# Kernel tuning notes

Hardware: AMD Instinct MI355X
Metric: run time of the kernel (lower is better)

## Reference

```python
import jax, jax.numpy as jnp
import numpy as np
import math

B, S, H, M, NH = 4, 1024, 1024, 32768, 1  # batch, seq, hidden, memory_size, num_heads


def setup_inputs() -> dict:
    key = jax.random.key(0)
    ks = jax.random.split(key, 12)
    init = lambda k, shape: (jax.random.normal(k, shape, dtype=jnp.float32) * 0.02)
    return {
        "hidden_states": jax.random.normal(ks[0], (B, S, H), dtype=jnp.float32),
        "Wq": init(ks[1], (H, H)), "bq": jnp.zeros((H,), jnp.float32),
        "Wk": init(ks[2], (H, H)), "bk": jnp.zeros((H,), jnp.float32),
        "Wv": init(ks[3], (H, H)), "bv": jnp.zeros((H,), jnp.float32),
        "Wo": init(ks[4], (H, H)), "bo": jnp.zeros((H,), jnp.float32),
        "memory_keys": init(ks[5], (NH, M, H)),
        "memory_values": init(ks[6], (NH, M, H)),
        "memory_age": jnp.zeros((NH, M), jnp.float32),
    }


def reference(hidden_states, Wq, bq, Wk, bk, Wv, bv, Wo, bo,
              memory_keys, memory_values, memory_age):
    b, s, _ = hidden_states.shape
    # projections (torch Linear: x @ W.T + b), split into heads
    q = (hidden_states @ Wq.T + bq).reshape(b, s, NH, -1)
    k = (hidden_states @ Wk.T + bk).reshape(b, s, NH, -1)
    v = (hidden_states @ Wv.T + bv).reshape(b, s, NH, -1)

    # cross-attention to external memory: [b,s,h,m]
    scores = jnp.einsum('bshd,hmd->bshm', q, memory_keys) / math.sqrt(H)
    probs = jax.nn.softmax(scores, axis=-1)  # dropout is identity (eval / p used deterministically)
    mem_out = jnp.einsum('bshm,hmd->bshd', probs, memory_values)

    # --- memory update (LRU-style topk scatter) ---
    age = memory_age + 1.0                       # [h,m]
    importance = probs.sum(axis=(0, 1))          # [h,m]
    _, upd_idx = jax.lax.top_k(age + (1.0 - importance), s)  # [h, s]
    h_idx = jnp.arange(NH)[:, None]              # [h,1]
    src_k = k[0, -1][:, None, :]                 # [h,1,d] -> broadcast over s slots
    src_v = v[0, -1][:, None, :]
    new_keys = memory_keys.at[h_idx, upd_idx].set(src_k)
    new_values = memory_values.at[h_idx, upd_idx].set(src_v)
    new_age = age.at[h_idx, upd_idx].set(0.0)

    output = mem_out.reshape(b, s, -1) @ Wo.T + bo

    access_counts = jnp.sum(probs > 0.01, axis=(0, 1))          # [h,m]
    max_scores = jnp.max(scores, axis=-1).mean()
    memory_usage = jnp.mean((new_age > 0).astype(jnp.float32))
    return (output, access_counts, max_scores, memory_usage,
            new_keys, new_values, new_age)
```

## Files before the change

kernel.cpp:

```cpp
#include <hip/hip_runtime.h>

#define SCALE 0.03125f
#define BAND_EPS 1e-6
#define BAND_CAP 8192
#define RB 4
#define NCHUNK 8

typedef unsigned int u32;
typedef unsigned short u16;
typedef unsigned long long u64;
typedef __attribute__((ext_vector_type(8))) short bf16x8;
typedef __attribute__((ext_vector_type(4))) float f32x4;

#define MFMA16(A,B,C) __builtin_amdgcn_mfma_f32_16x16x32_bf16(A,B,C,0,0,0)

__device__ __forceinline__ u32 fenc(float x){ u32 u=__float_as_uint(x); return (u&0x80000000u)? ~u : (u|0x80000000u); }
__device__ __forceinline__ float fdec(u32 e){ return (e&0x80000000u)? __uint_as_float(e&0x7FFFFFFFu) : __uint_as_float(~e); }
__device__ __forceinline__ u16 f2bf(float f){ u32 u=__float_as_uint(f); u32 r=(u + 0x7FFFu + ((u>>16)&1u))>>16; return (u16)r; }
__device__ __forceinline__ float bf2f(u16 h){ return __uint_as_float(((u32)h)<<16); }

__device__ __forceinline__ uint4 nt_load16(const void* p){
  const u64* q = (const u64*)p;
  u64 lo = __builtin_nontemporal_load(q);
  u64 hi = __builtin_nontemporal_load(q+1);
  uint4 r;
  r.x = (u32)lo; r.y = (u32)(lo>>32);
  r.z = (u32)hi; r.w = (u32)(hi>>32);
  return r;
}

__global__ __launch_bounds__(256) void k_projq64(const float* __restrict__ X, const float* __restrict__ W,
    const float* __restrict__ bias, float* __restrict__ Qhi, u16* __restrict__ Qh, u16* __restrict__ Ql)
{
  __shared__ float Xs[16][68], Ws[16][68];
  int t=threadIdx.x, ty=t>>4, tx=t&15;
  int row0=blockIdx.y*64, col0=blockIdx.x*64;
  int lr=t>>2, lk=(t&3)*4;
  double acc[4][4]={};
  for (int k0=0;k0<1024;k0+=16){
    __syncthreads();
    {
      float4 x = *(const float4*)(X + (size_t)(row0+lr)*1024 + k0 + lk);
      float4 w = *(const float4*)(W + (size_t)(col0+lr)*1024 + k0 + lk);
      Xs[lk+0][lr]=x.x; Xs[lk+1][lr]=x.y; Xs[lk+2][lr]=x.z; Xs[lk+3][lr]=x.w;
      Ws[lk+0][lr]=w.x; Ws[lk+1][lr]=w.y; Ws[lk+2][lr]=w.z; Ws[lk+3][lr]=w.w;
    }
    __syncthreads();
    #pragma unroll
    for (int kk=0;kk<16;kk++){
      double a[4], b[4];
      #pragma unroll
      for (int i=0;i<4;i++) a[i] = (double)Xs[kk][ty*4+i];
      #pragma unroll
      for (int j=0;j<4;j++) b[j] = (double)Ws[kk][tx*4+j];
      #pragma unroll
      for (int i=0;i<4;i++)
        #pragma unroll
        for (int j=0;j<4;j++)
          acc[i][j] = fma(a[i], b[j], acc[i][j]);
    }
  }
  #pragma unroll
  for (int i=0;i<4;i++)
    #pragma unroll
    for (int j=0;j<4;j++){
      double q = acc[i][j] + (double)bias[col0+tx*4+j];
      float hi = (float)q;
      size_t off = (size_t)(row0+ty*4+i)*1024 + col0 + tx*4 + j;
      Qhi[off] = hi;
      if (Qh){
        u16 h = f2bf(hi);
        Qh[off] = h;
        if (Ql) Ql[off] = f2bf(hi - bf2f(h));
      }
    }
}

__global__ __launch_bounds__(256) void k_rowproj(const float* __restrict__ hs,
    const float* __restrict__ Wk, const float* __restrict__ bk,
    const float* __restrict__ Wv, const float* __restrict__ bv,
    float* __restrict__ krow, float* __restrict__ vrow)
{
  int b = blockIdx.x; int which = b >> 10; int o = b & 1023; int t = threadIdx.x;
  const float* W = which ? Wv : Wk;
  const float* bias = which ? bv : bk;
  const float* x = hs + (size_t)1023*1024;
  double s = 0;
  for (int k=t;k<1024;k+=256) s += (double)x[k] * (double)W[(size_t)o*1024+k];
  __shared__ double sd[256];
  sd[t]=s; __syncthreads();
  for (int off=128;off>0;off>>=1){ if(t<off) sd[t]+=sd[t+off]; __syncthreads(); }
  if (t==0){ float* dst = which? vrow : krow; dst[o] = (float)(sd[0] + (double)bias[o]); }
}

__global__ __launch_bounds__(256) void k_cvt_mk(const float* __restrict__ src, u16* __restrict__ dst)
{
  size_t base = ((size_t)blockIdx.x*256 + threadIdx.x) * 16;
  float v[16];
  #pragma unroll
  for (int q=0;q<4;q++) *(float4*)&v[q*4] = *(const float4*)(src + base + q*4);
  u16 h[16];
  #pragma unroll
  for (int q=0;q<16;q++) h[q] = f2bf(v[q]);
  *(uint4*)(dst+base)   = *(uint4*)&h[0];
  *(uint4*)(dst+base+8) = *(uint4*)&h[8];
}

__global__ __launch_bounds__(256) void k_cvt_mvt(const float* __restrict__ MV, u32* __restrict__ MVT)
{
  size_t mp = blockIdx.x; int d = threadIdx.x*4;
  float4 r0 = *(const float4*)(MV + (2*mp  )*1024 + d);
  float4 r1 = *(const float4*)(MV + (2*mp+1)*1024 + d);
  u32 o[4];
  o[0] = (u32)f2bf(r0.x) | ((u32)f2bf(r1.x)<<16);
  o[1] = (u32)f2bf(r0.y) | ((u32)f2bf(r1.y)<<16);
  o[2] = (u32)f2bf(r0.z) | ((u32)f2bf(r1.z)<<16);
  o[3] = (u32)f2bf(r0.w) | ((u32)f2bf(r1.w)<<16);
  *(uint4*)(MVT + mp*1024 + d) = *(uint4*)o;
}

template<bool SPLIT>
__device__ __forceinline__ void sweep_core(
    const float* __restrict__ Qg, const float* __restrict__ MKg,
    int row0, int col0,
    u16 (*Ah)[40], u16 (*Al)[40], u16 (*Bh)[40],
    f32x4 acc[2][8])
{
  int t = threadIdx.x;
  int w = t >> 6, g = (t >> 4) & 3, c = t & 15;
  int srow = t >> 1, sq = (t & 1) * 16;
  const float* xg = Qg  + (size_t)(row0 + srow)*1024 + sq;
  const float* wg = MKg + (size_t)(col0 + srow)*1024 + sq;
  float xr[16], wr[16];
  #pragma unroll
  for (int q=0;q<4;q++){
    *(float4*)&xr[q*4] = *(const float4*)(xg + q*4);
    *(float4*)&wr[q*4] = *(const float4*)(wg + q*4);
  }
  for (int k0 = 0; k0 < 1024; k0 += 32){
    u16 ah[16], al[16], bh[16];
    #pragma unroll
    for (int q=0;q<16;q++){
      u16 h = f2bf(xr[q]); ah[q]=h;
      bh[q] = f2bf(wr[q]);
      if constexpr (SPLIT) al[q]=f2bf(xr[q]-bf2f(h));
    }
    __syncthreads();
    *(uint4*)&Ah[srow][sq]   = *(uint4*)&ah[0];
    *(uint4*)&Ah[srow][sq+8] = *(uint4*)&ah[8];
    *(uint4*)&Bh[srow][sq]   = *(uint4*)&bh[0];
    *(uint4*)&Bh[srow][sq+8] = *(uint4*)&bh[8];
    if constexpr (SPLIT){
      *(uint4*)&Al[srow][sq]   = *(uint4*)&al[0];
      *(uint4*)&Al[srow][sq+8] = *(uint4*)&al[8];
    }
    __syncthreads();
    if (k0 + 32 < 1024){
      #pragma unroll
      for (int q=0;q<4;q++){
        *(float4*)&xr[q*4] = *(const float4*)(xg + k0+32 + q*4);
        *(float4*)&wr[q*4] = *(const float4*)(wg + k0+32 + q*4);
      }
    }
    bf16x8 afh[2], afl[2];
    #pragma unroll
    for (int fi=0; fi<2; fi++){
      afh[fi] = *(const bf16x8*)&Ah[w*32 + fi*16 + c][g*8];
      if constexpr (SPLIT) afl[fi] = *(const bf16x8*)&Al[w*32 + fi*16 + c][g*8];
    }
    #pragma unroll
    for (int fj=0; fj<8; fj++){
      bf16x8 bfh = *(const bf16x8*)&Bh[fj*16 + c][g*8];
      #pragma unroll
      for (int fi=0; fi<2; fi++){
        acc[fi][fj] = MFMA16(afh[fi], bfh, acc[fi][fj]);
        if constexpr (SPLIT)
          acc[fi][fj] = MFMA16(afl[fi], bfh, acc[fi][fj]);
      }
    }
  }
}

template<bool SPLIT>
__device__ __forceinline__ void sweep_core_pre(
    const u16* __restrict__ Ag, const u16* __restrict__ Alg, const u16* __restrict__ Bg,
    int row0, int col0,
    u16 (*Ah)[40], u16 (*Al)[40], u16 (*Bh)[40],
    f32x4 acc[2][8])
{
  int t = threadIdx.x;
  int w = t >> 6, g = (t >> 4) & 3, c = t & 15;
  int srow = t >> 1, sq = (t & 1) * 16;
  const u16* xa = Ag + (size_t)(row0+srow)*1024 + sq;
  const u16* wb = Bg + (size_t)(col0+srow)*1024 + sq;
  const u16* xl = Alg + (size_t)(row0+srow)*1024 + sq;
  uint4 a0 = *(const uint4*)xa, a1 = *(const uint4*)(xa+8);
  uint4 b0 = *(const uint4*)wb, b1 = *(const uint4*)(wb+8);
  uint4 l0, l1;
  if constexpr (SPLIT){ l0 = *(const uint4*)xl; l1 = *(const uint4*)(xl+8); }
  for (int k0 = 0; k0 < 1024; k0 += 32){
    __syncthreads();
    *(uint4*)&Ah[srow][sq]   = a0;
    *(uint4*)&Ah[srow][sq+8] = a1;
    *(uint4*)&Bh[srow][sq]   = b0;
    *(uint4*)&Bh[srow][sq+8] = b1;
    if constexpr (SPLIT){
      *(uint4*)&Al[srow][sq]   = l0;
      *(uint4*)&Al[srow][sq+8] = l1;
    }
    __syncthreads();
    if (k0 + 32 < 1024){
      a0=*(const uint4*)(xa+k0+32); a1=*(const uint4*)(xa+k0+40);
      b0=*(const uint4*)(wb+k0+32); b1=*(const uint4*)(wb+k0+40);
      if constexpr (SPLIT){ l0=*(const uint4*)(xl+k0+32); l1=*(const uint4*)(xl+k0+40); }
    }
    bf16x8 afh[2], afl[2];
    #pragma unroll
    for (int fi=0; fi<2; fi++){
      afh[fi] = *(const bf16x8*)&Ah[w*32 + fi*16 + c][g*8];
      if constexpr (SPLIT) afl[fi] = *(const bf16x8*)&Al[w*32 + fi*16 + c][g*8];
    }
    #pragma unroll
    for (int fj=0; fj<8; fj++){
      bf16x8 bfh = *(const bf16x8*)&Bh[fj*16 + c][g*8];
      #pragma unroll
      for (int fi=0; fi<2; fi++){
        acc[fi][fj] = MFMA16(afh[fi], bfh, acc[fi][fj]);
        if constexpr (SPLIT)
          acc[fi][fj] = MFMA16(afl[fi], bfh, acc[fi][fj]);
      }
    }
  }
}

__device__ __forceinline__ void sweep1_epi(f32x4 acc[2][8], int row0,
    double* Zrow, u32* rmk)
{
  int t=threadIdx.x, w=t>>6, g=(t>>4)&3, c=t&15;
  #pragma unroll
  for (int fi=0;fi<2;fi++){
    #pragma unroll
    for (int r=0;r<4;r++){
      float mx=-1e30f, sm=0.f;
      #pragma unroll
      for (int fj=0;fj<8;fj++){
        float sc = acc[fi][fj][r]*SCALE;
        mx = fmaxf(mx, sc);
        sm += expf(sc);
      }
      #pragma unroll
      for (int o=1;o<16;o<<=1){
        mx = fmaxf(mx, __shfl_xor(mx,o,64));
        sm += __shfl_xor(sm,o,64);
      }
      if (c==0){
        int row = row0 + w*32 + fi*16 + g*4 + r;
        atomicMax(&rmk[row], fenc(mx));
        atomicAdd(&Zrow[row], (double)sm);
      }
    }
  }
}

__global__ __launch_bounds__(256) void k_sweep1m(const float* __restrict__ Q,
    const float* __restrict__ MK, double* __restrict__ Zrow, u32* __restrict__ rmk)
{
  __shared__ __align__(16) u16 ldsbuf[2*128*40];
  u16 (*Ah)[40]=(u16(*)[40])(ldsbuf);
  u16 (*Bh)[40]=(u16(*)[40])(ldsbuf+128*40);
  int row0=blockIdx.y*128, col0=blockIdx.x*128;
  f32x4 acc[2][8];
  #pragma unroll
  for (int fi=0;fi<2;fi++)
    #pragma unroll
    for (int fj=0;fj<8;fj++) acc[fi][fj] = (f32x4){0.f,0.f,0.f,0.f};
  sweep_core<false>(Q, MK, row0, col0, Ah, Ah, Bh, acc);
  sweep1_epi(acc, row0, Zrow, rmk);
}

__global__ __launch_bounds__(256) void k_sweep1p(const u16* __restrict__ Qh,
    const u16* __restrict__ MKh, double* __restrict__ Zrow, u32* __restrict__ rmk)
{
  __shared__ __align__(16) u16 ldsbuf[2*128*40];
  u16 (*Ah)[40]=(u16(*)[40])(ldsbuf);
  u16 (*Bh)[40]=(u16(*)[40])(ldsbuf+128*40);
  int row0=blockIdx.y*128, col0=blockIdx.x*128;
  f32x4 acc[2][8];
  #pragma unroll
  for (int fi=0;fi<2;fi++)
    #pragma unroll
    for (int fj=0;fj<8;fj++) acc[fi][fj] = (f32x4){0.f,0.f,0.f,0.f};
  sweep_core_pre<false>(Qh, Qh, MKh, row0, col0, Ah, Ah, Bh, acc);
  sweep1_epi(acc, row0, Zrow, rmk);
}

__global__ __launch_bounds__(256) void k_invz(const double* __restrict__ Z, const u32* __restrict__ rmk,
    float* __restrict__ invZ, double* __restrict__ invZd, float* __restrict__ rowmax)
{
  int r = blockIdx.x*256 + threadIdx.x;
  double iz = 1.0 / Z[r];
  invZ[r] = (float)iz;
  invZd[r] = iz;
  rowmax[r] = fdec(rmk[r]);
}

__device__ __forceinline__ void sweep2_epi(f32x4 acc[2][8], int row0, int col0,
    const float* invZ, double* imp, int* cnt, u16* P, u16* ldsbuf)
{
  int t=threadIdx.x, w=t>>6, g=(t>>4)&3, c=t&15;
  double colp[8]={0,0,0,0,0,0,0,0};
  int    colc[8]={0,0,0,0,0,0,0,0};
  #pragma unroll
  for (int fi=0;fi<2;fi++){
    float iz[4];
    #pragma unroll
    for (int r=0;r<4;r++) iz[r] = invZ[row0 + w*32 + fi*16 + g*4 + r];
    #pragma unroll
    for (int fj=0;fj<8;fj++){
      #pragma unroll
      for (int r=0;r<4;r++){
        float p = expf(acc[fi][fj][r]*SCALE)*iz[r];
        int row = row0 + w*32 + fi*16 + g*4 + r;
        __builtin_nontemporal_store(f2bf(p), &P[(size_t)row*32768 + col0 + fj*16 + c]);
        colp[fj] += (double)p;
        colc[fj] += (p > 0.01f) ? 1 : 0;
      }
    }
  }
  __syncthreads();
  double (*red)[128] = (double(*)[128])ldsbuf;
  #pragma unroll
  for (int fj=0;fj<8;fj++) red[w*4+g][fj*16+c] = colp[fj];
  __syncthreads();
  if (t < 128){
    double s=0;
    #pragma unroll
    for (int q=0;q<16;q++) s += red[q][t];
    atomicAdd(&imp[col0+t], s);
  }
  __syncthreads();
  #pragma unroll
  for (int fj=0;fj<8;fj++) red[w*4+g][fj*16+c] = (double)colc[fj];
  __syncthreads();
  if (t < 128){
    double s=0;
    #pragma unroll
    for (int q=0;q<16;q++) s += red[q][t];
    int ci = (int)(s+0.5);
    if (ci) atomicAdd(&cnt[col0+t], ci);
  }
}

__global__ __launch_bounds__(256) void k_sweep2m(const float* __restrict__ Q,
    const float* __restrict__ MK, const float* __restrict__ invZ,
    double* __restrict__ imp, int* __restrict__ cnt, u16* __restrict__ P)
{
  __shared__ __align__(16) u16 ldsbuf[3*128*40];
  u16 (*Ah)[40]=(u16(*)[40])(ldsbuf);
  u16 (*Al)[40]=(u16(*)[40])(ldsbuf+128*40);
  u16 (*Bh)[40]=(u16(*)[40])(ldsbuf+2*128*40);
  int row0=blockIdx.y*128, col0=blockIdx.x*128;
  f32x4 acc[2][8];
  #pragma unroll
  for (int fi=0;fi<2;fi++)
    #pragma unroll
    for (int fj=0;fj<8;fj++) acc[fi][fj] = (f32x4){0.f,0.f,0.f,0.f};
  sweep_core<true>(Q, MK, row0, col0, Ah, Al, Bh, acc);
  sweep2_epi(acc, row0, col0, invZ, imp, cnt, P, ldsbuf);
}

__global__ __launch_bounds__(256) void k_sweep2p(const u16* __restrict__ Qh,
    const u16* __restrict__ MKh, const float* __restrict__ invZ,
    double* __restrict__ imp, int* __restrict__ cnt, u16* __restrict__ P)
{
  __shared__ __align__(16) u16 ldsbuf[2*128*40];
  u16 (*Ah)[40]=(u16(*)[40])(ldsbuf);
  u16 (*Bh)[40]=(u16(*)[40])(ldsbuf+128*40);
  int row0=blockIdx.y*128, col0=blockIdx.x*128;
  f32x4 acc[2][8];
  #pragma unroll
  for (int fi=0;fi<2;fi++)
    #pragma unroll
    for (int fj=0;fj<8;fj++) acc[fi][fj] = (f32x4){0.f,0.f,0.f,0.f};
  sweep_core_pre<false>(Qh, Qh, MKh, row0, col0, Ah, Ah, Bh, acc);
  sweep2_epi(acc, row0, col0, invZ, imp, cnt, P, ldsbuf);
}

template<int MODE>
__global__ __launch_bounds__(1024) void k_select(const double* __restrict__ imp,
    const float* __restrict__ mage, double* __restrict__ vsout, int* __restrict__ sel)
{
  __shared__ int hist[256];
  __shared__ int scanbuf[1024];
  __shared__ u32 s_digit; __shared__ int s_rr;
  int t = threadIdx.x;
  int m0 = t*32;
  u32 key[32];
  #pragma unroll
  for (int i=0;i<32;i++){
    int m = m0+i;
    float v = (mage[m] + 1.0f) + (1.0f - (float)imp[m]);
    key[i] = fenc(v);
  }
  u32 prefix = 0, pmask = 0;
  int rr = 1024;
  for (int pass=0; pass<4; pass++){
    int shift = 24 - pass*8;
    if (t<256) hist[t]=0;
    __syncthreads();
    #pragma unroll
    for (int i=0;i<32;i++){
      if ((key[i] & pmask) == prefix)
        atomicAdd(&hist[(key[i]>>shift)&255u], 1);
    }
    __syncthreads();
    if (t==0){
      int cum=0; int d=255;
      for (; d>0; d--){
        if (cum + hist[d] >= rr) break;
        cum += hist[d];
      }
      s_rr = rr - cum;
      s_digit = (u32)d;
    }
    __syncthreads();
    rr = s_rr;
    prefix |= (s_digit << shift);
    pmask  |= (255u << shift);
    __syncthreads();
  }
  u32 keystar = prefix;
  int krem = rr;
  if (MODE==0){
    if (t==0) *vsout = (double)fdec(keystar);
    return;
  }
  int lc = 0;
  #pragma unroll
  for (int i=0;i<32;i++) lc += (key[i]==keystar) ? 1 : 0;
  scanbuf[t] = lc;
  __syncthreads();
  for (int off=1; off<1024; off<<=1){
    int v_ = scanbuf[t];
    int add = (t>=off)? scanbuf[t-off] : 0;
    __syncthreads();
    scanbuf[t] = v_ + add;
    __syncthreads();
  }
  int run = scanbuf[t] - lc;
  #pragma unroll
  for (int i=0;i<32;i++){
    int s_;
    if (key[i] > keystar) s_ = 1;
    else if (key[i] == keystar){ s_ = (run < krem) ? 1 : 0; run++; }
    else s_ = 0;
    sel[m0+i] = s_;
  }
}

__global__ __launch_bounds__(256) void k_band(const double* __restrict__ imp,
    const float* __restrict__ mage, const double* __restrict__ vsp,
    int* __restrict__ bandcnt, int* __restrict__ bandidx)
{
  int m = blockIdx.x*256 + threadIdx.x;
  double v = ((double)mage[m] + 1.0) + (1.0 - imp[m]);
  double vs = *vsp;
  if (fabs(v - vs) <= BAND_EPS){
    int idx = atomicAdd(bandcnt, 1);
    if (idx < BAND_CAP) bandidx[idx] = m;
  }
}

__global__ __launch_bounds__(256) void k_repair2(const int* __restrict__ bandcnt, const int* __restrict__ bandidx,
    const float* __restrict__ Qhi, const float* __restrict__ MK,
    const double* __restrict__ invZd, double* __restrict__ partial)
{
  int bc = *bandcnt; if (bc > BAND_CAP) bc = BAND_CAP;
  int s0 = blockIdx.x * RB;
  if (s0 >= bc) return;
  int ns = bc - s0; if (ns > RB) ns = RB;
  int r0 = blockIdx.y * 512;
  __shared__ float mks[RB][1024];
  __shared__ double izl[512];
  __shared__ double red[256];
  int t = threadIdx.x;
  for (int idx = t; idx < RB*1024; idx += 256){
    int j = idx >> 10, d = idx & 1023;
    mks[j][d] = (j < ns) ? MK[(size_t)bandidx[s0+j]*1024 + d] : 0.f;
  }
  for (int r = t; r < 512; r += 256) izl[r] = invZd[r0 + r];
  __syncthreads();
  int wave = t>>6, lane = t&63, d0 = lane*16, sl = lane&3;
  double mkr[RB][16];
  #pragma unroll
  for (int j=0;j<RB;j++)
    #pragma unroll
    for (int q=0;q<16;q++) mkr[j][q] = (double)mks[j][d0+q];
  double acc = 0;
  for (int rr = wave; rr < 512; rr += 4){
    const float4* hp = (const float4*)(Qhi + (size_t)(r0+rr)*1024 + d0);
    float4 h0=hp[0], h1=hp[1], h2=hp[2], h3=hp[3];
    double hh[16]={h0.x,h0.y,h0.z,h0.w,h1.x,h1.y,h1.z,h1.w,
                   h2.x,h2.y,h2.z,h2.w,h3.x,h3.y,h3.z,h3.w};
    double p[RB];
    #pragma unroll
    for (int j=0;j<RB;j++){
      double a0=0, a1=0;
      #pragma unroll
      for (int q=0;q<8;q++){
        a0 = fma(hh[2*q],   mkr[j][2*q],   a0);
        a1 = fma(hh[2*q+1], mkr[j][2*q+1], a1);
      }
      p[j] = a0 + a1;
    }
    #pragma unroll
    for (int o=1;o<16;o<<=1)
      #pragma unroll
      for (int j=0;j<RB;j++) p[j] += __shfl_xor(p[j], o, 64);
    double v = (sl==0)? p[0] : (sl==1)? p[1] : (sl==2)? p[2] : p[3];
    v += __shfl_xor(v, 16, 64);
    v += __shfl_xor(v, 32, 64);
    acc += exp(v * (1.0/32.0)) * izl[rr];
  }
  red[t] = acc;
  __syncthreads();
  for (int o=128; o>=RB; o>>=1){
    if (t < o) red[t] += red[t+o];
    __syncthreads();
  }
  if (t < ns) partial[(size_t)(s0+t)*NCHUNK + blockIdx.y] = red[t];
}

__global__ __launch_bounds__(256) void k_repair_fin(const int* __restrict__ bandcnt,
    const int* __restrict__ bandidx, const double* __restrict__ partial, double* __restrict__ imp)
{
  int bc = *bandcnt; if (bc > BAND_CAP) bc = BAND_CAP;
  int slot = blockIdx.x*256 + threadIdx.x;
  if (slot >= bc) return;
  double s = 0;
  #pragma unroll
  for (int ch=0; ch<NCHUNK; ch++) s += partial[(size_t)slot*NCHUNK + ch];
  imp[bandidx[slot]] = s * 0.0625;
}

__global__ __launch_bounds__(256) void k_pvm(const u16* __restrict__ P,
    const float* __restrict__ MV, float* __restrict__ O)
{
  __shared__ __align__(16) u16 Ap[128][40];
  __shared__ u32 Bv[16][132];
  int t=threadIdx.x, w=t>>6, g=(t>>4)&3, c=t&15;
  int row0=blockIdx.x*128, d0=blockIdx.y*128;
  size_t kb0 = (size_t)blockIdx.z*8192;
  int srow=t>>1, sq=(t&1)*16;
  int mp=t>>5, dc=t&31;
  f32x4 acc[2][8];
  #pragma unroll
  for (int fi=0;fi<2;fi++)
    #pragma unroll
    for (int fj=0;fj<8;fj++) acc[fi][fj] = (f32x4){0.f,0.f,0.f,0.f};
  const u16*  pg  = P  + (size_t)(row0+srow)*32768 + kb0 + sq;
  const float* mva = MV + (kb0 + 2*mp  )*1024 + d0 + dc;
  const float* mvb = mva + 1024;
  const float* mvc = mva + 16*1024;
  const float* mvd = mvc + 1024;
  uint4 pa0 = *(const uint4*)pg;
  uint4 pa1 = *(const uint4*)(pg + 8);
  float a0[4], b0[4], a1[4], b1[4];
  #pragma unroll
  for (int j=0;j<4;j++){ a0[j]=mva[32*j]; b0[j]=mvb[32*j]; a1[j]=mvc[32*j]; b1[j]=mvd[32*j]; }
  for (int kt=0; kt<256; kt++){
    __syncthreads();
    *(uint4*)&Ap[srow][sq]   = pa0;
    *(uint4*)&Ap[srow][sq+8] = pa1;
    #pragma unroll
    for (int j=0;j<4;j++){
      Bv[mp  ][dc+32*j] = (u32)f2bf(a0[j]) | ((u32)f2bf(b0[j])<<16);
      Bv[mp+8][dc+32*j] = (u32)f2bf(a1[j]) | ((u32)f2bf(b1[j])<<16);
    }
    __syncthreads();
    if (kt+1 < 256){
      size_t ko = (size_t)(kt+1)*32;
      pa0 = *(const uint4*)(pg + ko);
      pa1 = *(const uint4*)(pg + ko + 8);
      size_t fo = ko*1024;
      #pragma unroll
      for (int j=0;j<4;j++){
        a0[j]=mva[fo+32*j]; b0[j]=mvb[fo+32*j];
        a1[j]=mvc[fo+32*j]; b1[j]=mvd[fo+32*j];
      }
    }
    bf16x8 af[2];
    af[0] = *(const bf16x8*)&Ap[w*32 + c][g*8];
    af[1] = *(const bf16x8*)&Ap[w*32 + 16 + c][g*8];
    #pragma unroll
    for (int fj=0; fj<8; fj++){
      union { u32 u[4]; bf16x8 v; } bb;
      #pragma unroll
      for (int qq=0; qq<4; qq++) bb.u[qq] = Bv[4*g+qq][fj*16 + c];
      acc[0][fj] = MFMA16(af[0], bb.v, acc[0][fj]);
      acc[1][fj] = MFMA16(af[1], bb.v, acc[1][fj]);
    }
  }
  #pragma unroll
  for (int fi=0;fi<2;fi++)
    #pragma unroll
    for (int fj=0;fj<8;fj++)
      #pragma unroll
      for (int r=0;r<4;r++)
        atomicAdd(&O[(size_t)(row0 + w*32 + fi*16 + g*4 + r)*1024 + d0 + fj*16 + c],
                  acc[fi][fj][r]);
}

__global__ __launch_bounds__(256) void k_pvmp(const u16* __restrict__ P,
    const u32* __restrict__ MVT, float* __restrict__ O)
{
  __shared__ __align__(16) u16 Ap[128][40];
  __shared__ u32 Bv[16][132];
  int t=threadIdx.x, w=t>>6, g=(t>>4)&3, c=t&15;
  int row0=blockIdx.x*128, d0=blockIdx.y*128;
  size_t kb0 = (size_t)blockIdx.z*8192;
  size_t pb0 = kb0 >> 1;
  int srow=t>>1, sq=(t&1)*16;
  int mp=t>>5, dc=t&31;
  f32x4 acc[2][8];
  #pragma unroll
  for (int fi=0;fi<2;fi++)
    #pragma unroll
    for (int fj=0;fj<8;fj++) acc[fi][fj] = (f32x4){0.f,0.f,0.f,0.f};
  const u16* pg   = P   + (size_t)(row0+srow)*32768 + kb0 + sq;
  const u32* mvt0 = MVT + (pb0 + mp    )*1024 + d0 + dc;
  const u32* mvt1 = MVT + (pb0 + 8 + mp)*1024 + d0 + dc;
  uint4 pa0 = nt_load16(pg);
  uint4 pa1 = nt_load16(pg + 8);
  u32 b0[4], b1[4];
  #pragma unroll
  for (int j=0;j<4;j++){ b0[j]=mvt0[32*j]; b1[j]=mvt1[32*j]; }
  for (int kt=0; kt<256; kt++){
    __syncthreads();
    *(uint4*)&Ap[srow][sq]   = pa0;
    *(uint4*)&Ap[srow][sq+8] = pa1;
    #pragma unroll
    for (int j=0;j<4;j++){
      Bv[mp  ][dc+32*j] = b0[j];
      Bv[mp+8][dc+32*j] = b1[j];
    }
    __syncthreads();
    if (kt+1 < 256){
      size_t ko = (size_t)(kt+1)*32;
      pa0 = nt_load16(pg + ko);
      pa1 = nt_load16(pg + ko + 8);
      size_t fo = (size_t)(kt+1)*16*1024;
      #pragma unroll
      for (int j=0;j<4;j++){ b0[j]=mvt0[fo+32*j]; b1[j]=mvt1[fo+32*j]; }
    }
    bf16x8 af[2];
    af[0] = *(const bf16x8*)&Ap[w*32 + c][g*8];
    af[1] = *(const bf16x8*)&Ap[w*32 + 16 + c][g*8];
    #pragma unroll
    for (int fj=0; fj<8; fj++){
      union { u32 u[4]; bf16x8 v; } bb;
      #pragma unroll
      for (int qq=0; qq<4; qq++) bb.u[qq] = Bv[4*g+qq][fj*16 + c];
      acc[0][fj] = MFMA16(af[0], bb.v, acc[0][fj]);
      acc[1][fj] = MFMA16(af[1], bb.v, acc[1][fj]);
    }
  }
  #pragma unroll
  for (int fi=0;fi<2;fi++)
    #pragma unroll
    for (int fj=0;fj<8;fj++)
      #pragma unroll
      for (int r=0;r<4;r++)
        atomicAdd(&O[(size_t)(row0 + w*32 + fi*16 + g*4 + r)*1024 + d0 + fj*16 + c],
                  acc[fi][fj][r]);
}

__global__ __launch_bounds__(256) void k_projm(const float* __restrict__ X,
    const float* __restrict__ W, const float* __restrict__ bias, float* __restrict__ Y)
{
  __shared__ __align__(16) u16 ldsbuf[2*128*40];
  u16 (*Ah)[40]=(u16(*)[40])(ldsbuf);
  u16 (*Bh)[40]=(u16(*)[40])(ldsbuf+128*40);
  int t=threadIdx.x, w=t>>6, g=(t>>4)&3, c=t&15;
  int row0=blockIdx.y*128, col0=blockIdx.x*128;
  f32x4 acc[2][8];
  #pragma unroll
  for (int fi=0;fi<2;fi++)
    #pragma unroll
    for (int fj=0;fj<8;fj++) acc[fi][fj] = (f32x4){0.f,0.f,0.f,0.f};
  sweep_core<false>(X, W, row0, col0, Ah, Ah, Bh, acc);
  #pragma unroll
  for (int fi=0;fi<2;fi++)
    #pragma unroll
    for (int fj=0;fj<8;fj++){
      float bb = bias[col0 + fj*16 + c];
      #pragma unroll
      for (int r=0;r<4;r++)
        Y[(size_t)(row0 + w*32 + fi*16 + g*4 + r)*1024 + col0 + fj*16 + c]
          = acc[fi][fj][r] + bb;
    }
}

__global__ __launch_bounds__(256) void k_scatter(const float* __restrict__ mk, const float* __restrict__ mv,
    const float* __restrict__ mage, const float* __restrict__ krow, const float* __restrict__ vrow,
    const int* __restrict__ sel, float* __restrict__ nk, float* __restrict__ nv,
    float* __restrict__ na, int* __restrict__ usage)
{
  int s = blockIdx.x, t = threadIdx.x;
  bool is = sel[s] != 0;
  const float2* sk = (const float2*)krow;
  const float2* sv = (const float2*)vrow;
  const float2* ok = (const float2*)(mk + (size_t)s*1024);
  const float2* ov = (const float2*)(mv + (size_t)s*1024);
  float2* dk = (float2*)(nk + (size_t)s*1024);
  float2* dv = (float2*)(nv + (size_t)s*1024);
  #pragma unroll
  for (int q=t;q<512;q+=256){
    dk[q] = is ? sk[q] : ok[q];
    dv[q] = is ? sv[q] : ov[q];
  }
  if (t==0){
    float a = mage[s] + 1.0f;
    float nav = is ? 0.0f : a;
    na[s] = nav;
    if (nav > 0.0f) atomicAdd(usage, 1);
  }
}

__global__ __launch_bounds__(256) void k_fin(const float* __restrict__ rowmax, const int* __restrict__ cnt,
    const int* __restrict__ usage, float* __restrict__ acc_out, float* __restrict__ scal)
{
  int t = threadIdx.x;
  __shared__ double sd[256];
  double s = 0;
  for (int r=t;r<4096;r+=256) s += (double)rowmax[r];
  sd[t]=s; __syncthreads();
  for (int o=128;o>0;o>>=1){ if (t<o) sd[t]+=sd[t+o]; __syncthreads(); }
  if (t==0){
    scal[0] = (float)(sd[0] / 4096.0);
    scal[1] = (float)((double)(*usage) / 32768.0);
  }
  for (int m=t;m<32768;m+=256) acc_out[m] = (float)cnt[m];
}

extern "C" void kernel_launch(void* const* d_in, const int* in_sizes, int n_in,
                              void* d_out, int out_size, void* d_ws, size_t ws_size,
                              hipStream_t stream) {
  const float* hs  = (const float*)d_in[0];
  const float* Wq  = (const float*)d_in[1];
  const float* bq  = (const float*)d_in[2];
  const float* Wk  = (const float*)d_in[3];
  const float* bk  = (const float*)d_in[4];
  const float* Wv  = (const float*)d_in[5];
  const float* bv  = (const float*)d_in[6];
  const float* Wo  = (const float*)d_in[7];
  const float* bo  = (const float*)d_in[8];
  const float* mk  = (const float*)d_in[9];
  const float* mv  = (const float*)d_in[10];
  const float* mage= (const float*)d_in[11];
  float* out = (float*)d_out;

  char* ws = (char*)d_ws;
  const size_t MB = 1024*1024;
  bool fast = ws_size >= 82*MB;
  size_t stats_off = fast ? 80*MB : 16*MB;
  char* st = ws + stats_off;

  double* Zrow   = (double*)(st);
  u32*    rmk    = (u32*)  (st + 32768);
  float*  invZ   = (float*)(st + 49152);
  double* invZd  = (double*)(st + 65536);
  float*  rowmax = (float*)(st + 98304);
  double* imp    = (double*)(st + 114688);
  int*    cnt    = (int*)  (st + 376832);
  int*    sel    = (int*)  (st + 507904);
  float*  krow   = (float*)(st + 638976);
  float*  vrow   = (float*)(st + 643072);
  int*    usage  = (int*)  (st + 647168);
  double* vstar  = (double*)(st + 647176);
  int*    bandcnt= (int*)  (st + 647184);
  int*    bandidx= (int*)  (st + 647188);
  double* partial= (double*)(st + 680960);

  float* O   = (float*)ws;
  u16*   Qh  = (u16*)ws;
  u16*   MKh = (u16*)(ws + 16*MB);
  u32*   MVT = (u32*)(ws + 16*MB);

  float* Qhi = (float*)d_out;
  u16*   P   = (u16*)((char*)d_out + 16908544);

  dim3 blk(256);
  if (fast){
    hipMemsetAsync(st, 0, 647188 + BAND_CAP*4, stream);
    k_projq64<<<dim3(16,64),blk,0,stream>>>(hs, Wq, bq, Qhi, Qh, nullptr);
    k_cvt_mk<<<8192,blk,0,stream>>>(mk, MKh);
    k_rowproj<<<2048,blk,0,stream>>>(hs, Wk, bk, Wv, bv, krow, vrow);
    k_sweep1p<<<dim3(256,32),blk,0,stream>>>(Qh, MKh, Zrow, rmk);
    k_invz<<<16,blk,0,stream>>>(Zrow, rmk, invZ, invZd, rowmax);
    k_sweep2p<<<dim3(256,32),blk,0,stream>>>(Qh, MKh, invZ, imp, cnt, P);
    hipMemsetAsync(ws, 0, 16*MB, stream);
    k_cvt_mvt<<<16384,blk,0,stream>>>(mv, MVT);
    k_select<0><<<1,1024,0,stream>>>(imp, mage, vstar, nullptr);
    k_band<<<128,blk,0,stream>>>(imp, mage, vstar, bandcnt, bandidx);
    k_repair2<<<dim3(BAND_CAP/RB, NCHUNK),blk,0,stream>>>(bandcnt, bandidx, Qhi, mk, invZd, partial);
    k_repair_fin<<<BAND_CAP/256,blk,0,stream>>>(bandcnt, bandidx, partial, imp);
    k_pvmp<<<dim3(32,8,4),blk,0,stream>>>(P, MVT, O);
    k_projm<<<dim3(8,32),blk,0,stream>>>(O, Wo, bo, out);
    k_select<1><<<1,1024,0,stream>>>(imp, mage, nullptr, sel);
    k_scatter<<<32768,blk,0,stream>>>(mk, mv, mage, krow, vrow, sel,
        out + 4227074, out + 37781506, out + 71335938, usage);
    k_fin<<<1,blk,0,stream>>>(rowmax, cnt, usage, out + 4194304, out + 4227072);
  } else {
    hipMemsetAsync(ws, 0, 16*MB + 647188 + BAND_CAP*4, stream);
    k_projq64<<<dim3(16,64),blk,0,stream>>>(hs, Wq, bq, Qhi, nullptr, nullptr);
    k_rowproj<<<2048,blk,0,stream>>>(hs, Wk, bk, Wv, bv, krow, vrow);
    k_sweep1m<<<dim3(256,32),blk,0,stream>>>(Qhi, mk, Zrow, rmk);
    k_invz<<<16,blk,0,stream>>>(Zrow, rmk, invZ, invZd, rowmax);
    k_sweep2m<<<dim3(256,32),blk,0,stream>>>(Qhi, mk, invZ, imp, cnt, P);
    k_select<0><<<1,1024,0,stream>>>(imp, mage, vstar, nullptr);
    k_band<<<128,blk,0,stream>>>(imp, mage, vstar, bandcnt, bandidx);
    k_repair2<<<dim3(BAND_CAP/RB, NCHUNK),blk,0,stream>>>(bandcnt, bandidx, Qhi, mk, invZd, partial);
    k_repair_fin<<<BAND_CAP/256,blk,0,stream>>>(bandcnt, bandidx, partial, imp);
    k_pvm<<<dim3(32,8,4),blk,0,stream>>>(P, mv, O);
    k_projm<<<dim3(8,32),blk,0,stream>>>(O, Wo, bo, out);
    k_select<1><<<1,1024,0,stream>>>(imp, mage, nullptr, sel);
    k_scatter<<<32768,blk,0,stream>>>(mk, mv, mage, krow, vrow, sel,
        out + 4227074, out + 37781506, out + 71335938, usage);
    k_fin<<<1,blk,0,stream>>>(rowmax, cnt, usage, out + 4194304, out + 4227072);
  }
}
```

Measured before the change: 2.735 ms.

## Double-buffer LDS tiles in P·V memory GEMM with two-stage prefetch

```diff
diff --git a/kernel.cpp b/kernel.cpp
--- a/kernel.cpp
+++ b/kernel.cpp
@@ -614,8 +614,10 @@
 __global__ __launch_bounds__(256) void k_pvmp(const u16* __restrict__ P,
     const u32* __restrict__ MVT, float* __restrict__ O)
 {
-  __shared__ __align__(16) u16 Ap[128][40];
-  __shared__ u32 Bv[16][132];
+  __shared__ __align__(16) u16 Ap0[128][40];
+  __shared__ __align__(16) u16 Ap1[128][40];
+  __shared__ u32 Bv0[16][132];
+  __shared__ u32 Bv1[16][132];
   int t=threadIdx.x, w=t>>6, g=(t>>4)&3, c=t&15;
   int row0=blockIdx.x*128, d0=blockIdx.y*128;
   size_t kb0 = (size_t)blockIdx.z*8192;
@@ -630,41 +632,55 @@
   const u16* pg   = P   + (size_t)(row0+srow)*32768 + kb0 + sq;
   const u32* mvt0 = MVT + (pb0 + mp    )*1024 + d0 + dc;
   const u32* mvt1 = MVT + (pb0 + 8 + mp)*1024 + d0 + dc;
-  uint4 pa0 = nt_load16(pg);
-  uint4 pa1 = nt_load16(pg + 8);
-  u32 b0[4], b1[4];
-  #pragma unroll
-  for (int j=0;j<4;j++){ b0[j]=mvt0[32*j]; b1[j]=mvt1[32*j]; }
-  for (int kt=0; kt<256; kt++){
-    __syncthreads();
-    *(uint4*)&Ap[srow][sq]   = pa0;
-    *(uint4*)&Ap[srow][sq+8] = pa1;
-    #pragma unroll
-    for (int j=0;j<4;j++){
-      Bv[mp  ][dc+32*j] = b0[j];
-      Bv[mp+8][dc+32*j] = b1[j];
-    }
-    __syncthreads();
-    if (kt+1 < 256){
-      size_t ko = (size_t)(kt+1)*32;
-      pa0 = nt_load16(pg + ko);
-      pa1 = nt_load16(pg + ko + 8);
-      size_t fo = (size_t)(kt+1)*16*1024;
-      #pragma unroll
-      for (int j=0;j<4;j++){ b0[j]=mvt0[fo+32*j]; b1[j]=mvt1[fo+32*j]; }
-    }
-    bf16x8 af[2];
-    af[0] = *(const bf16x8*)&Ap[w*32 + c][g*8];
-    af[1] = *(const bf16x8*)&Ap[w*32 + 16 + c][g*8];
-    #pragma unroll
-    for (int fj=0; fj<8; fj++){
-      union { u32 u[4]; bf16x8 v; } bb;
-      #pragma unroll
-      for (int qq=0; qq<4; qq++) bb.u[qq] = Bv[4*g+qq][fj*16 + c];
-      acc[0][fj] = MFMA16(af[0], bb.v, acc[0][fj]);
-      acc[1][fj] = MFMA16(af[1], bb.v, acc[1][fj]);
-    }
-  }
+
+  uint4 paA0, paA1, paB0, paB1;
+  u32 vbA0[4], vbA1[4], vbB0[4], vbB1[4];
+  #define LOAD_A(kt) { size_t ko=(size_t)(kt)*32; \
+    paA0 = nt_load16(pg + ko); paA1 = nt_load16(pg + ko + 8); \
+    size_t fo=(size_t)(kt)*16*1024; \
+    _Pragma("unroll") for (int j=0;j<4;j++){ vbA0[j]=mvt0[fo+32*j]; vbA1[j]=mvt1[fo+32*j]; } }
+  #define LOAD_B(kt) { size_t ko=(size_t)(kt)*32; \
+    paB0 = nt_load16(pg + ko); paB1 = nt_load16(pg + ko + 8); \
+    size_t fo=(size_t)(kt)*16*1024; \
+    _Pragma("unroll") for (int j=0;j<4;j++){ vbB0[j]=mvt0[fo+32*j]; vbB1[j]=mvt1[fo+32*j]; } }
+  #define WRITE0_A() { *(uint4*)&Ap0[srow][sq]=paA0; *(uint4*)&Ap0[srow][sq+8]=paA1; \
+    _Pragma("unroll") for (int j=0;j<4;j++){ Bv0[mp][dc+32*j]=vbA0[j]; Bv0[mp+8][dc+32*j]=vbA1[j]; } }
+  #define WRITE1_B() { *(uint4*)&Ap1[srow][sq]=paB0; *(uint4*)&Ap1[srow][sq+8]=paB1; \
+    _Pragma("unroll") for (int j=0;j<4;j++){ Bv1[mp][dc+32*j]=vbB0[j]; Bv1[mp+8][dc+32*j]=vbB1[j]; } }
+  #define WRITE0_B() { *(uint4*)&Ap0[srow][sq]=paB0; *(uint4*)&Ap0[srow][sq+8]=paB1; \
+    _Pragma("unroll") for (int j=0;j<4;j++){ Bv0[mp][dc+32*j]=vbB0[j]; Bv0[mp+8][dc+32*j]=vbB1[j]; } }
+  #define WRITE1_A() { *(uint4*)&Ap1[srow][sq]=paA0; *(uint4*)&Ap1[srow][sq+8]=paA1; \
+    _Pragma("unroll") for (int j=0;j<4;j++){ Bv1[mp][dc+32*j]=vbA0[j]; Bv1[mp+8][dc+32*j]=vbA1[j]; } }
+  #define DO_MFMA(AP, BV) { \
+    bf16x8 af0 = *(const bf16x8*)&AP[w*32 + c][g*8]; \
+    bf16x8 af1 = *(const bf16x8*)&AP[w*32 + 16 + c][g*8]; \
+    _Pragma("unroll") for (int fj=0; fj<8; fj++){ \
+      union { u32 u[4]; bf16x8 v; } bb; \
+      _Pragma("unroll") for (int qq=0; qq<4; qq++) bb.u[qq] = BV[4*g+qq][fj*16 + c]; \
+      acc[0][fj] = MFMA16(af0, bb.v, acc[0][fj]); \
+      acc[1][fj] = MFMA16(af1, bb.v, acc[1][fj]); } }
+
+  LOAD_A(0);
+  LOAD_B(1);
+  WRITE0_A();
+  __syncthreads();
+  for (int kt=0; kt<256; kt+=2){
+    if (kt+2 < 256) LOAD_A(kt+2);
+    WRITE1_B();
+    DO_MFMA(Ap0, Bv0);
+    __syncthreads();
+    if (kt+3 < 256) LOAD_B(kt+3);
+    if (kt+2 < 256) WRITE0_A();
+    DO_MFMA(Ap1, Bv1);
+    __syncthreads();
+  }
+  #undef LOAD_A
+  #undef LOAD_B
+  #undef WRITE0_A
+  #undef WRITE1_B
+  #undef WRITE0_B
+  #undef WRITE1_A
+  #undef DO_MFMA
   #pragma unroll
   for (int fi=0;fi<2;fi++)
     #pragma unroll
```

After: 2.753 ms. Within noise of the previous version (+0.7%).
